# Kernel tuning notes

Measured on AMD Instinct MI355X. Metric: run time of the kernel, lower is better.

## Reference

```python
import jax, jax.numpy as jnp
import numpy as np

D_MODEL = 1280
NUM_EXPERTS = 20
HEAD_DIM = D_MODEL // NUM_EXPERTS  # 64
SCALE = HEAD_DIM ** -0.5


def setup_inputs() -> dict:
    key = jax.random.key(0)
    ks = jax.random.split(key, 8)
    B, S = 4, 1024
    s_in = 1.0 / np.sqrt(D_MODEL)
    x = jax.random.normal(ks[0], (B, S, D_MODEL), dtype=jnp.float32)
    # per-expert QKV projections stacked: [E, d_model, 3*head_dim]
    wqkv = jax.random.uniform(ks[1], (NUM_EXPERTS, D_MODEL, 3 * HEAD_DIM), jnp.float32, -s_in, s_in)
    bqkv = jax.random.uniform(ks[2], (NUM_EXPERTS, 3 * HEAD_DIM), jnp.float32, -s_in, s_in)
    router_w = jax.random.uniform(ks[3], (D_MODEL, NUM_EXPERTS), jnp.float32, -s_in, s_in)
    router_b = jax.random.uniform(ks[4], (NUM_EXPERTS,), jnp.float32, -s_in, s_in)
    out_w = jax.random.uniform(ks[5], (D_MODEL, D_MODEL), jnp.float32, -s_in, s_in)
    out_b = jax.random.uniform(ks[6], (D_MODEL,), jnp.float32, -s_in, s_in)
    return {"x": x, "wqkv": wqkv, "bqkv": bqkv, "router_w": router_w,
            "router_b": router_b, "out_w": out_w, "out_b": out_b}


def reference(x, wqkv, bqkv, router_w, router_b, out_w, out_b):
    # x: [B, S, D]
    B, S, D = x.shape
    E, H = NUM_EXPERTS, HEAD_DIM
    # router softmax gates (dropout = identity in eval)
    gates = jax.nn.softmax(x @ router_w + router_b, axis=-1)  # [B, S, E]
    # per-expert QKV: [E, B, S, 3H]
    qkv = jnp.einsum('bsd,edh->ebsh', x, wqkv) + bqkv[:, None, None, :]
    q, k, v = jnp.split(qkv, 3, axis=-1)  # each [E, B, S, H]
    scores = jnp.einsum('ebqh,ebkh->ebqk', q, k) * SCALE  # [E, B, S, S]
    attn = jax.nn.softmax(scores, axis=-1)
    eo = jnp.einsum('ebqk,ebkh->ebqh', attn, v)  # [E, B, S, H]
    # gate multiply and scatter into disjoint feature slices == concat over experts
    eo = eo * jnp.transpose(gates, (2, 0, 1))[..., None]  # [E, B, S, H]
    combined = jnp.transpose(eo, (1, 2, 0, 3)).reshape(B, S, E * H)  # [B, S, D]
    return combined @ out_w + out_b
```

## Files before the change

### kernel.cpp

```cpp
#include <hip/hip_runtime.h>
#include <hip/hip_bf16.h>

#define D_MODEL 1280
#define NUM_EXPERTS 20
#define HEAD_DIM 64
#define SEQ 1024
#define BATCH 4
#define BS_TOK 4096
#define QKV_N 192
#define QKV_W 3840

typedef __attribute__((ext_vector_type(8))) short short8;
typedef __attribute__((ext_vector_type(4))) float f32x4;
typedef __attribute__((ext_vector_type(16))) float f32x16;
typedef __hip_bfloat16 bf16;

static __device__ __forceinline__ void gload_lds16(const void* g, void* l) {
  __builtin_amdgcn_global_load_lds((const __attribute__((address_space(1))) void*)g,
                                   (__attribute__((address_space(3))) void*)l, 16, 0, 0);
}

__global__ __launch_bounds__(256) void k_rwT(const float* __restrict__ in,
                                             float* __restrict__ out) {
  int i = blockIdx.x * 256 + threadIdx.x;
  if (i < D_MODEL * NUM_EXPERTS) {
    int d = i / NUM_EXPERTS, e = i % NUM_EXPERTS;
    out[e * D_MODEL + d] = in[i];
  }
}

__global__ __launch_bounds__(256) void k_gates(const float* __restrict__ x,
    const float* __restrict__ rwT, const float* __restrict__ rb,
    float* __restrict__ gates, bf16* __restrict__ xb)
{
  __shared__ float xs[4][D_MODEL];
  __shared__ float logits[4][NUM_EXPERTS];
  const int r0 = blockIdx.x * 4;
  for (int i = threadIdx.x; i < 4 * (D_MODEL / 2); i += 256) {
    int r = i / (D_MODEL / 2), d2 = (i % (D_MODEL / 2)) * 2;
    float2 v = *(const float2*)(x + (size_t)(r0 + r) * D_MODEL + d2);
    xs[r][d2] = v.x; xs[r][d2 + 1] = v.y;
    __hip_bfloat162 h;
    h.x = __float2bfloat16(v.x); h.y = __float2bfloat16(v.y);
    *(__hip_bfloat162*)(xb + (size_t)(r0 + r) * D_MODEL + d2) = h;
  }
  __syncthreads();
  const int wid = threadIdx.x >> 6, lane = threadIdx.x & 63;
  for (int e = 0; e < NUM_EXPERTS; ++e) {
    float s = 0.f;
    #pragma unroll
    for (int j = 0; j < D_MODEL / 64; ++j) {
      int d = lane + 64 * j;
      s += xs[wid][d] * rwT[e * D_MODEL + d];
    }
    #pragma unroll
    for (int m = 32; m >= 1; m >>= 1) s += __shfl_xor(s, m);
    if (lane == 0) logits[wid][e] = s + rb[e];
  }
  __syncthreads();
  if (lane < 32) {
    float v = (lane < NUM_EXPERTS) ? logits[wid][lane] : -1e30f;
    float mx = v;
    #pragma unroll
    for (int m = 16; m >= 1; m >>= 1) mx = fmaxf(mx, __shfl_xor(mx, m, 32));
    float p = (lane < NUM_EXPERTS) ? __expf(v - mx) : 0.f;
    float sum = p;
    #pragma unroll
    for (int m = 16; m >= 1; m >>= 1) sum += __shfl_xor(sum, m, 32);
    if (lane < NUM_EXPERTS)
      gates[(size_t)(r0 + wid) * NUM_EXPERTS + lane] = p / sum;
  }
}

__global__ __launch_bounds__(256) void k_transpose(const float* __restrict__ in,
    bf16* __restrict__ out, int R, int C)
{
  __shared__ float tile[32][33];
  const size_t bo = (size_t)blockIdx.z * R * C;
  const int c0 = blockIdx.x * 32, r0 = blockIdx.y * 32;
  const int tx = threadIdx.x, ty = threadIdx.y;
  #pragma unroll
  for (int i = 0; i < 4; ++i)
    tile[ty + 8*i][tx] = in[bo + (size_t)(r0 + ty + 8*i) * C + (c0 + tx)];
  __syncthreads();
  #pragma unroll
  for (int i = 0; i < 4; ++i)
    out[bo + (size_t)(c0 + ty + 8*i) * R + (r0 + tx)] =
        __float2bfloat16(tile[tx][ty + 8*i]);
}

__global__ __launch_bounds__(512, 2) void k_gemm256(
    const bf16* __restrict__ A, const bf16* __restrict__ BT,
    const float* __restrict__ bias, bf16* __restrict__ C,
    int M, int N, int K)
{
  __shared__ __align__(16) bf16 lds[4][2][256 * 32];
  const int bid = blockIdx.x;
  const int xcd = bid & 7, c = bid >> 3;
  const int m0 = (xcd * 2 + (c & 1)) * 256;
  const int n0 = (c >> 1) * 256;
  const int tid = threadIdx.x, wid = tid >> 6, lane = tid & 63;
  const int wr = wid >> 2, wcn = wid & 3;
  const int fr = lane & 15, fg = lane >> 4;
  const int nt = K / 32;

  auto STAGE = [&](int t, int buf) {
    const bf16* Ag = A + (size_t)m0 * K + t * 32;
    const bf16* Bg = BT + (size_t)n0 * K + t * 32;
    #pragma unroll
    for (int i = 0; i < 2; ++i) {
      int idx = i * 512 + tid;
      int row = idx >> 2, sc = idx & 3;
      int g = sc ^ (row & 3);
      gload_lds16(Ag + (size_t)row * K + g * 8, &lds[buf][0][idx * 8]);
    }
    #pragma unroll
    for (int i = 0; i < 2; ++i) {
      int idx = i * 512 + tid;
      int row = idx >> 2, sc = idx & 3;
      int g = sc ^ (row & 3);
      gload_lds16(Bg + (size_t)row * K + g * 8, &lds[buf][1][idx * 8]);
    }
  };

  f32x4 acc[8][4] = {};
  auto COMPUTE = [&](int buf) {
    const bf16* As_ = &lds[buf][0][0];
    const bf16* Bs_ = &lds[buf][1][0];
    short8 af[8], bfv[4];
    #pragma unroll
    for (int mi = 0; mi < 8; ++mi) {
      int row = wr * 128 + mi * 16 + fr;
      int slot = fg ^ (row & 3);
      af[mi] = *(const short8*)(As_ + row * 32 + slot * 8);
    }
    #pragma unroll
    for (int ni = 0; ni < 4; ++ni) {
      int row = wcn * 64 + ni * 16 + fr;
      int slot = fg ^ (row & 3);
      bfv[ni] = *(const short8*)(Bs_ + row * 32 + slot * 8);
    }
    __builtin_amdgcn_s_setprio(1);
    #pragma unroll
    for (int mi = 0; mi < 8; ++mi) {
      #pragma unroll
      for (int ni = 0; ni < 4; ++ni)
        acc[mi][ni] = __builtin_amdgcn_mfma_f32_16x16x32_bf16(
            af[mi], bfv[ni], acc[mi][ni], 0, 0, 0);
    }
    __builtin_amdgcn_s_setprio(0);
  };

  STAGE(0, 0); STAGE(1, 1); STAGE(2, 2);
  asm volatile("s_waitcnt vmcnt(8)" ::: "memory");
  __builtin_amdgcn_s_barrier();
  __builtin_amdgcn_sched_barrier(0);
  int buf = 0;
  for (int t = 0; t < nt - 3; ++t) {
    int nb = buf + 3; nb = (nb >= 4) ? nb - 4 : nb;
    STAGE(t + 3, nb);
    COMPUTE(buf);
    asm volatile("s_waitcnt vmcnt(8)" ::: "memory");
    __builtin_amdgcn_s_barrier();
    __builtin_amdgcn_sched_barrier(0);
    buf = (buf == 3) ? 0 : buf + 1;
  }
  COMPUTE(buf);
  asm volatile("s_waitcnt vmcnt(4)" ::: "memory");
  __builtin_amdgcn_s_barrier();
  __builtin_amdgcn_sched_barrier(0);
  buf = (buf == 3) ? 0 : buf + 1;
  COMPUTE(buf);
  asm volatile("s_waitcnt vmcnt(0)" ::: "memory");
  __builtin_amdgcn_s_barrier();
  __builtin_amdgcn_sched_barrier(0);
  buf = (buf == 3) ? 0 : buf + 1;
  COMPUTE(buf);

  #pragma unroll
  for (int mi = 0; mi < 8; ++mi) {
    const int gr = m0 + wr * 128 + mi * 16 + fg * 4;
    #pragma unroll
    for (int ni = 0; ni < 4; ++ni) {
      const int gc = n0 + wcn * 64 + ni * 16 + fr;
      const float bv = bias[gc];
      #pragma unroll
      for (int r = 0; r < 4; ++r)
        C[(size_t)(gr + r) * N + gc] = __float2bfloat16(acc[mi][ni][r] + bv);
    }
  }
}

template<bool OUT_BF16>
__global__ __launch_bounds__(256) void k_gemm(
    const bf16* __restrict__ A, const bf16* __restrict__ BT,
    const float* __restrict__ bias, void* __restrict__ C,
    int M, int N, int K)
{
  __shared__ __align__(16) bf16 As[128 * 64];
  __shared__ __align__(16) bf16 Bs[128 * 64];
  const int bid = blockIdx.x;
  const int xcd = bid & 7, c = bid >> 3;
  const int m0 = (xcd * 4 + (c & 3)) * 128;
  const int n0 = (c >> 2) * 128;
  const int tid = threadIdx.x, wid = tid >> 6, lane = tid & 63;
  const int wr = wid >> 1, wc = wid & 1;
  const int fr = lane & 15, fg = lane >> 4;
  f32x4 acc[4][4] = {};
  for (int k0 = 0; k0 < K; k0 += 64) {
    #pragma unroll
    for (int p = 0; p < 4; ++p) {
      int eidx = ((p*4 + wid)*64 + lane) * 8;
      int row = eidx >> 6, col = eidx & 63;
      gload_lds16(A + (size_t)(m0 + row)*K + k0 + col, As + eidx);
      gload_lds16(BT + (size_t)(n0 + row)*K + k0 + col, Bs + eidx);
    }
    __syncthreads();
    short8 af[2][4], bfr[2][4];
    #pragma unroll
    for (int kk = 0; kk < 2; ++kk) {
      #pragma unroll
      for (int mi = 0; mi < 4; ++mi)
        af[kk][mi] = *(const short8*)(As + (wr*64 + mi*16 + fr)*64 + kk*32 + fg*8);
      #pragma unroll
      for (int ni = 0; ni < 4; ++ni)
        bfr[kk][ni] = *(const short8*)(Bs + (wc*64 + ni*16 + fr)*64 + kk*32 + fg*8);
    }
    #pragma unroll
    for (int kk = 0; kk < 2; ++kk) {
      #pragma unroll
      for (int mi = 0; mi < 4; ++mi) {
        #pragma unroll
        for (int ni = 0; ni < 4; ++ni)
          acc[mi][ni] = __builtin_amdgcn_mfma_f32_16x16x32_bf16(
              af[kk][mi], bfr[kk][ni], acc[mi][ni], 0, 0, 0);
      }
    }
    __syncthreads();
  }
  #pragma unroll
  for (int mi = 0; mi < 4; ++mi) {
    const int gr = m0 + wr*64 + mi*16 + fg*4;
    #pragma unroll
    for (int ni = 0; ni < 4; ++ni) {
      const int gc = n0 + wc*64 + ni*16 + fr;
      const float bv = bias[gc];
      #pragma unroll
      for (int r = 0; r < 4; ++r) {
        float v = acc[mi][ni][r] + bv;
        size_t off = (size_t)(gr + r) * N + gc;
        if constexpr (OUT_BF16) ((bf16*)C)[off] = __float2bfloat16(v);
        else                    ((float*)C)[off] = v;
      }
    }
  }
}

__global__ __launch_bounds__(256, 4) void k_attn(
    const bf16* __restrict__ qkv, const float* __restrict__ gates,
    bf16* __restrict__ combined)
{
  __shared__ __align__(16) bf16 Ks[2][64 * 64];
  __shared__ __align__(16) bf16 VTs[2][64 * 64];
  __shared__ float Ltab[64];
  const int id = blockIdx.x;
  const int xcd = id & 7, kgrp = id >> 3;
  const int qt = kgrp / 10, bel = kgrp - qt * 10;
  const int be = xcd * 10 + bel;
  const int e = be >> 2, b = be & 3;
  const int s0 = qt * 64;
  const int tid = threadIdx.x, wid = tid >> 6, lane = tid & 63;
  const int l31 = lane & 31, hi = lane >> 5;
  const int qw = wid & 1, kh = wid >> 1;
  const bf16* base = qkv + (size_t)(b * SEQ) * QKV_W + e * QKV_N;
  const int rq = s0 + qw * 32 + l31;
  short8 qf[4];
  #pragma unroll
  for (int kc = 0; kc < 4; ++kc)
    qf[kc] = *(const short8*)(base + (size_t)rq * QKV_W + kc*16 + hi*8);
  f32x16 o0 = {}, o1 = {};
  float Lr = 0.f;
  const float CSC = 0.125f * 1.44269504f;

  const int kst_row = (lane >> 3);
  short8 vreg[2];
  auto KSTAGE = [&](int c0, int bsel) {
    #pragma unroll
    for (int p = 0; p < 2; ++p) {
      int W = p*4 + wid;
      int row = W*8 + kst_row;
      int g = (lane & 7) ^ W ^ kst_row;
      gload_lds16(base + (size_t)(c0 + row)*QKV_W + 64 + g*8,
                  &Ks[bsel][(W*64 + lane)*8]);
    }
  };
  auto VLOAD = [&](int c0) {
    #pragma unroll
    for (int it = 0; it < 2; ++it) {
      int key = it*32 + (tid >> 3);
      vreg[it] = *(const short8*)(base + (size_t)(c0 + key)*QKV_W + 128 + (tid & 7)*8);
    }
  };
  auto VWRITE = [&](int bsel) {
    #pragma unroll
    for (int it = 0; it < 2; ++it) {
      int key = it*32 + (tid >> 3);
      int h0b = tid & 7;
      int kc_ = key >> 3, ko = key & 7;
      union { short8 v; bf16 hh[8]; } u; u.v = vreg[it];
      #pragma unroll
      for (int j = 0; j < 8; ++j) {
        int scn = kc_ ^ h0b ^ j;
        VTs[bsel][(h0b*8 + j)*64 + scn*8 + ko] = u.hh[j];
      }
    }
  };

  KSTAGE(0, 0); VLOAD(0);
  int bsel = 0;
  const int krow = kh*32 + l31;
  const int Sk = ((krow >> 3) ^ krow) & 7;
  for (int t = 0; t < SEQ / 64; ++t) {
    VWRITE(bsel);
    __syncthreads();
    if (t < SEQ / 64 - 1) { KSTAGE((t + 1) * 64, bsel ^ 1); VLOAD((t + 1) * 64); }
    f32x16 sc = {};
    __builtin_amdgcn_s_setprio(1);
    #pragma unroll
    for (int kc = 0; kc < 4; ++kc) {
      int st = (kc*2 + hi) ^ Sk;
      short8 kf = *(const short8*)(&Ks[bsel][krow*64 + st*8]);
      sc = __builtin_amdgcn_mfma_f32_32x32x16_bf16(kf, qf[kc], sc, 0, 0, 0);
    }
    __builtin_amdgcn_s_setprio(0);
    float p[16]; float ls = 0.f;
    #pragma unroll
    for (int i = 0; i < 16; ++i) { p[i] = exp2f(sc[i]*CSC); ls += p[i]; }
    Lr += ls + __shfl_xor(ls, 32);
    union { int w[4]; short8 v; } pf0, pf1;
    int ta, tb;
    asm("v_cvt_pk_bf16_f32 %0, %1, %2" : "=v"(ta) : "v"(p[0]), "v"(p[1]));
    asm("v_cvt_pk_bf16_f32 %0, %1, %2" : "=v"(tb) : "v"(p[4]), "v"(p[5]));
    asm volatile("v_permlane32_swap_b32 %0, %1" : "+v"(ta), "+v"(tb));
    pf0.w[0] = ta; pf0.w[2] = tb;
    asm("v_cvt_pk_bf16_f32 %0, %1, %2" : "=v"(ta) : "v"(p[2]), "v"(p[3]));
    asm("v_cvt_pk_bf16_f32 %0, %1, %2" : "=v"(tb) : "v"(p[6]), "v"(p[7]));
    asm volatile("v_permlane32_swap_b32 %0, %1" : "+v"(ta), "+v"(tb));
    pf0.w[1] = ta; pf0.w[3] = tb;
    asm("v_cvt_pk_bf16_f32 %0, %1, %2" : "=v"(ta) : "v"(p[8]), "v"(p[9]));
    asm("v_cvt_pk_bf16_f32 %0, %1, %2" : "=v"(tb) : "v"(p[12]), "v"(p[13]));
    asm volatile("v_permlane32_swap_b32 %0, %1" : "+v"(ta), "+v"(tb));
    pf1.w[0] = ta; pf1.w[2] = tb;
    asm("v_cvt_pk_bf16_f32 %0, %1, %2" : "=v"(ta) : "v"(p[10]), "v"(p[11]));
    asm("v_cvt_pk_bf16_f32 %0, %1, %2" : "=v"(tb) : "v"(p[14]), "v"(p[15]));
    asm volatile("v_permlane32_swap_b32 %0, %1" : "+v"(ta), "+v"(tb));
    pf1.w[1] = ta; pf1.w[3] = tb;
    __builtin_amdgcn_s_setprio(1);
    #pragma unroll
    for (int kb = 0; kb < 2; ++kb) {
      const short8 pv = (kb == 0) ? pf0.v : pf1.v;
      #pragma unroll
      for (int hb = 0; hb < 2; ++hb) {
        int h = hb*32 + l31;
        int cc = (kh*4 + kb*2 + hi) ^ (((h >> 3) ^ h) & 7);
        short8 vf = *(const short8*)(&VTs[bsel][h*64 + cc*8]);
        if (hb == 0) o0 = __builtin_amdgcn_mfma_f32_32x32x16_bf16(pv, vf, o0, 0, 0, 0);
        else         o1 = __builtin_amdgcn_mfma_f32_32x32x16_bf16(pv, vf, o1, 0, 0, 0);
      }
    }
    __builtin_amdgcn_s_setprio(0);
    bsel ^= 1;
  }
  __syncthreads();
  float* Ops = (float*)&Ks[0][0];
  float* Lp  = (float*)&VTs[0][0];
  if (kh == 1) {
    #pragma unroll
    for (int reg = 0; reg < 16; ++reg) {
      int crow = (reg & 3) + 8*(reg >> 2) + 4*hi;
      Ops[(qw*32 + crow)*64 + l31]      = o0[reg];
      Ops[(qw*32 + crow)*64 + 32 + l31] = o1[reg];
    }
    if (lane < 32) Lp[qw*32 + lane] = Lr;
  }
  __syncthreads();
  if (kh == 0) {
    #pragma unroll
    for (int reg = 0; reg < 16; ++reg) {
      int crow = (reg & 3) + 8*(reg >> 2) + 4*hi;
      o0[reg] += Ops[(qw*32 + crow)*64 + l31];
      o1[reg] += Ops[(qw*32 + crow)*64 + 32 + l31];
    }
    if (lane < 32) {
      float Lt = Lr + Lp[qw*32 + lane];
      float g = gates[(size_t)(b*SEQ + s0 + qw*32 + lane) * NUM_EXPERTS + e];
      Ltab[qw*32 + lane] = g / Lt;
    }
    const int rowbase = b*SEQ + s0 + qw*32;
    #pragma unroll
    for (int reg = 0; reg < 16; ++reg) {
      int crow = (reg & 3) + 8*(reg >> 2) + 4*hi;
      float inv = Ltab[qw*32 + crow];
      combined[(size_t)(rowbase + crow)*D_MODEL + e*64 + l31] =
          __float2bfloat16(o0[reg] * inv);
      combined[(size_t)(rowbase + crow)*D_MODEL + e*64 + 32 + l31] =
          __float2bfloat16(o1[reg] * inv);
    }
  }
}

extern "C" void kernel_launch(void* const* d_in, const int* in_sizes, int n_in,
                              void* d_out, int out_size, void* d_ws, size_t ws_size,
                              hipStream_t stream) {
  const float* x    = (const float*)d_in[0];
  const float* wqkv = (const float*)d_in[1];
  const float* bqkv = (const float*)d_in[2];
  const float* rw   = (const float*)d_in[3];
  const float* rb   = (const float*)d_in[4];
  const float* ow   = (const float*)d_in[5];
  const float* ob   = (const float*)d_in[6];
  char* ws = (char*)d_ws;
  bf16*  xb    = (bf16*)(ws);
  bf16*  wqkvT = (bf16*)(ws + 10485760);
  bf16*  owT   = (bf16*)(ws + 20316160);
  float* gates = (float*)(ws + 23592960);
  bf16*  qkv   = (bf16*)(ws + 23920640);
  bf16*  comb  = (bf16*)(ws + 55377920);
  float* rwT   = (float*)comb;

  k_rwT<<<(D_MODEL * NUM_EXPERTS + 255) / 256, 256, 0, stream>>>(rw, rwT);
  k_gates<<<1024, 256, 0, stream>>>(x, rwT, rb, gates, xb);
  k_transpose<<<dim3(6, 40, 20), dim3(32, 8), 0, stream>>>(wqkv, wqkvT, D_MODEL, QKV_N);
  k_transpose<<<dim3(40, 40, 1), dim3(32, 8), 0, stream>>>(ow, owT, D_MODEL, D_MODEL);
  k_gemm256<<<240, 512, 0, stream>>>(xb, wqkvT, bqkv, qkv, BS_TOK, QKV_W, D_MODEL);
  k_attn<<<1280, 256, 0, stream>>>(qkv, gates, comb);
  k_gemm<false><<<8 * 4 * (D_MODEL / 128), 256, 0, stream>>>(comb, owT, ob, d_out,
                                                             BS_TOK, D_MODEL, D_MODEL);
}
```

Baseline: 165.0 us.

## Pipeline output GEMM with 4-stage LDS ring and shrink attention V buffer

Replaces the simple synchronous output-projection GEMM with a 512-thread kernel that stages K=32 slices into a 4-deep LDS ring with swizzled addressing. It waits on partial vmcnt so global loads overlap with MFMA work. Separately, the attention kernel drops V-transpose double buffering to a single buffer with an extra barrier, cutting LDS use to raise occupancy at the cost of one more sync per tile.

Result: faster. 156.2 us (-5.4%).

```diff
diff --git a/kernel.cpp b/kernel.cpp
--- a/kernel.cpp
+++ b/kernel.cpp
@@ -191,67 +191,94 @@
   }
 }
 
-template<bool OUT_BF16>
-__global__ __launch_bounds__(256) void k_gemm(
+__global__ __launch_bounds__(512, 2) void k_gemm128r(
     const bf16* __restrict__ A, const bf16* __restrict__ BT,
-    const float* __restrict__ bias, void* __restrict__ C,
+    const float* __restrict__ bias, float* __restrict__ C,
     int M, int N, int K)
 {
-  __shared__ __align__(16) bf16 As[128 * 64];
-  __shared__ __align__(16) bf16 Bs[128 * 64];
+  __shared__ __align__(16) bf16 lds[4][2][128 * 32];
   const int bid = blockIdx.x;
   const int xcd = bid & 7, c = bid >> 3;
   const int m0 = (xcd * 4 + (c & 3)) * 128;
   const int n0 = (c >> 2) * 128;
   const int tid = threadIdx.x, wid = tid >> 6, lane = tid & 63;
-  const int wr = wid >> 1, wc = wid & 1;
+  const int wr = wid >> 2, wcn = wid & 3;
   const int fr = lane & 15, fg = lane >> 4;
-  f32x4 acc[4][4] = {};
-  for (int k0 = 0; k0 < K; k0 += 64) {
-    #pragma unroll
-    for (int p = 0; p < 4; ++p) {
-      int eidx = ((p*4 + wid)*64 + lane) * 8;
-      int row = eidx >> 6, col = eidx & 63;
-      gload_lds16(A + (size_t)(m0 + row)*K + k0 + col, As + eidx);
-      gload_lds16(BT + (size_t)(n0 + row)*K + k0 + col, Bs + eidx);
-    }
-    __syncthreads();
-    short8 af[2][4], bfr[2][4];
-    #pragma unroll
-    for (int kk = 0; kk < 2; ++kk) {
-      #pragma unroll
-      for (int mi = 0; mi < 4; ++mi)
-        af[kk][mi] = *(const short8*)(As + (wr*64 + mi*16 + fr)*64 + kk*32 + fg*8);
-      #pragma unroll
-      for (int ni = 0; ni < 4; ++ni)
-        bfr[kk][ni] = *(const short8*)(Bs + (wc*64 + ni*16 + fr)*64 + kk*32 + fg*8);
-    }
-    #pragma unroll
-    for (int kk = 0; kk < 2; ++kk) {
-      #pragma unroll
-      for (int mi = 0; mi < 4; ++mi) {
-        #pragma unroll
-        for (int ni = 0; ni < 4; ++ni)
-          acc[mi][ni] = __builtin_amdgcn_mfma_f32_16x16x32_bf16(
-              af[kk][mi], bfr[kk][ni], acc[mi][ni], 0, 0, 0);
-      }
-    }
-    __syncthreads();
-  }
+  const int nt = K / 32;
+
+  auto STAGE = [&](int t, int buf) {
+    const bf16* Ag = A + (size_t)m0 * K + t * 32;
+    const bf16* Bg = BT + (size_t)n0 * K + t * 32;
+    int row = tid >> 2, sc = tid & 3;
+    int g = sc ^ (row & 3);
+    gload_lds16(Ag + (size_t)row * K + g * 8, &lds[buf][0][tid * 8]);
+    gload_lds16(Bg + (size_t)row * K + g * 8, &lds[buf][1][tid * 8]);
+  };
+
+  f32x4 acc[4][2] = {};
+  auto COMPUTE = [&](int buf) {
+    const bf16* As_ = &lds[buf][0][0];
+    const bf16* Bs_ = &lds[buf][1][0];
+    short8 af[4], bfv[2];
+    #pragma unroll
+    for (int mi = 0; mi < 4; ++mi) {
+      int row = wr * 64 + mi * 16 + fr;
+      int slot = fg ^ (row & 3);
+      af[mi] = *(const short8*)(As_ + row * 32 + slot * 8);
+    }
+    #pragma unroll
+    for (int ni = 0; ni < 2; ++ni) {
+      int row = wcn * 32 + ni * 16 + fr;
+      int slot = fg ^ (row & 3);
+      bfv[ni] = *(const short8*)(Bs_ + row * 32 + slot * 8);
+    }
+    __builtin_amdgcn_s_setprio(1);
+    #pragma unroll
+    for (int mi = 0; mi < 4; ++mi) {
+      #pragma unroll
+      for (int ni = 0; ni < 2; ++ni)
+        acc[mi][ni] = __builtin_amdgcn_mfma_f32_16x16x32_bf16(
+            af[mi], bfv[ni], acc[mi][ni], 0, 0, 0);
+    }
+    __builtin_amdgcn_s_setprio(0);
+  };
+
+  STAGE(0, 0); STAGE(1, 1); STAGE(2, 2);
+  asm volatile("s_waitcnt vmcnt(4)" ::: "memory");
+  __builtin_amdgcn_s_barrier();
+  __builtin_amdgcn_sched_barrier(0);
+  int buf = 0;
+  for (int t = 0; t < nt - 3; ++t) {
+    int nb = buf + 3; nb = (nb >= 4) ? nb - 4 : nb;
+    STAGE(t + 3, nb);
+    COMPUTE(buf);
+    asm volatile("s_waitcnt vmcnt(4)" ::: "memory");
+    __builtin_amdgcn_s_barrier();
+    __builtin_amdgcn_sched_barrier(0);
+    buf = (buf == 3) ? 0 : buf + 1;
+  }
+  COMPUTE(buf);
+  asm volatile("s_waitcnt vmcnt(2)" ::: "memory");
+  __builtin_amdgcn_s_barrier();
+  __builtin_amdgcn_sched_barrier(0);
+  buf = (buf == 3) ? 0 : buf + 1;
+  COMPUTE(buf);
+  asm volatile("s_waitcnt vmcnt(0)" ::: "memory");
+  __builtin_amdgcn_s_barrier();
+  __builtin_amdgcn_sched_barrier(0);
+  buf = (buf == 3) ? 0 : buf + 1;
+  COMPUTE(buf);
+
   #pragma unroll
   for (int mi = 0; mi < 4; ++mi) {
-    const int gr = m0 + wr*64 + mi*16 + fg*4;
-    #pragma unroll
-    for (int ni = 0; ni < 4; ++ni) {
-      const int gc = n0 + wc*64 + ni*16 + fr;
+    const int gr = m0 + wr * 64 + mi * 16 + fg * 4;
+    #pragma unroll
+    for (int ni = 0; ni < 2; ++ni) {
+      const int gc = n0 + wcn * 32 + ni * 16 + fr;
       const float bv = bias[gc];
       #pragma unroll
-      for (int r = 0; r < 4; ++r) {
-        float v = acc[mi][ni][r] + bv;
-        size_t off = (size_t)(gr + r) * N + gc;
-        if constexpr (OUT_BF16) ((bf16*)C)[off] = __float2bfloat16(v);
-        else                    ((float*)C)[off] = v;
-      }
+      for (int r = 0; r < 4; ++r)
+        C[(size_t)(gr + r) * N + gc] = acc[mi][ni][r] + bv;
     }
   }
 }
@@ -261,7 +288,7 @@
     bf16* __restrict__ combined)
 {
   __shared__ __align__(16) bf16 Ks[2][64 * 64];
-  __shared__ __align__(16) bf16 VTs[2][64 * 64];
+  __shared__ __align__(16) bf16 VTs[64 * 64];
   __shared__ float Ltab[64];
   const int id = blockIdx.x;
   const int xcd = id & 7, kgrp = id >> 3;
@@ -301,7 +328,7 @@
       vreg[it] = *(const short8*)(base + (size_t)(c0 + key)*QKV_W + 128 + (tid & 7)*8);
     }
   };
-  auto VWRITE = [&](int bsel) {
+  auto VWRITE = [&]() {
     #pragma unroll
     for (int it = 0; it < 2; ++it) {
       int key = it*32 + (tid >> 3);
@@ -311,7 +338,7 @@
       #pragma unroll
       for (int j = 0; j < 8; ++j) {
         int scn = kc_ ^ h0b ^ j;
-        VTs[bsel][(h0b*8 + j)*64 + scn*8 + ko] = u.hh[j];
+        VTs[(h0b*8 + j)*64 + scn*8 + ko] = u.hh[j];
       }
     }
   };
@@ -321,7 +348,8 @@
   const int krow = kh*32 + l31;
   const int Sk = ((krow >> 3) ^ krow) & 7;
   for (int t = 0; t < SEQ / 64; ++t) {
-    VWRITE(bsel);
+    if (t) __syncthreads();
+    VWRITE();
     __syncthreads();
     if (t < SEQ / 64 - 1) { KSTAGE((t + 1) * 64, bsel ^ 1); VLOAD((t + 1) * 64); }
     f32x16 sc = {};
@@ -363,7 +391,7 @@
       for (int hb = 0; hb < 2; ++hb) {
         int h = hb*32 + l31;
         int cc = (kh*4 + kb*2 + hi) ^ (((h >> 3) ^ h) & 7);
-        short8 vf = *(const short8*)(&VTs[bsel][h*64 + cc*8]);
+        short8 vf = *(const short8*)(&VTs[h*64 + cc*8]);
         if (hb == 0) o0 = __builtin_amdgcn_mfma_f32_32x32x16_bf16(pv, vf, o0, 0, 0, 0);
         else         o1 = __builtin_amdgcn_mfma_f32_32x32x16_bf16(pv, vf, o1, 0, 0, 0);
       }
@@ -373,7 +401,7 @@
   }
   __syncthreads();
   float* Ops = (float*)&Ks[0][0];
-  float* Lp  = (float*)&VTs[0][0];
+  float* Lp  = (float*)&VTs[0];
   if (kh == 1) {
     #pragma unroll
     for (int reg = 0; reg < 16; ++reg) {
@@ -434,6 +462,6 @@
   k_transpose<<<dim3(40, 40, 1), dim3(32, 8), 0, stream>>>(ow, owT, D_MODEL, D_MODEL);
   k_gemm256<<<240, 512, 0, stream>>>(xb, wqkvT, bqkv, qkv, BS_TOK, QKV_W, D_MODEL);
   k_attn<<<1280, 256, 0, stream>>>(qkv, gates, comb);
-  k_gemm<false><<<8 * 4 * (D_MODEL / 128), 256, 0, stream>>>(comb, owT, ob, d_out,
-                                                             BS_TOK, D_MODEL, D_MODEL);
-}
+  k_gemm128r<<<320, 512, 0, stream>>>(comb, owT, ob, (float*)d_out,
+                                      BS_TOK, D_MODEL, D_MODEL);
+}
```
